# Optimization experiments

Hardware: AMD Instinct MI355X
Metric: run time of the kernel (lower is better)

## Reference

```python
import jax, jax.numpy as jnp
import numpy as np

B, IN_C, OUT_C, H, W = 16, 64, 64, 128, 128
MIN_R, MAX_R, BASE, SCALE = 1, 6, 3, 3


def setup_inputs() -> dict:
    key = jax.random.key(0)
    k1, k2 = jax.random.split(key)
    x = jax.random.normal(k1, (B, IN_C, H, W), dtype=jnp.float32)
    # kaiming-uniform-ish scale for a 3x3 conv weight
    weight = jax.random.normal(k2, (OUT_C, IN_C, 3, 3), dtype=jnp.float32) * (1.0 / np.sqrt(IN_C * 9))
    # truncated-normal-style integer dilation per output channel (deterministic)
    rng = np.random.default_rng(0)
    offsets = np.clip(np.round(rng.normal(BASE, SCALE, size=OUT_C)), MIN_R, MAX_R).astype(np.int32)
    return {"x": x, "weight": weight, "offsets": offsets}


def _gsd_conv(x, weight, offs_np):
    # Per-channel dilation conv: group channels by dilation, conv each group
    # (dilation=o, padding=o keeps HxW), scatter back to original channel order.
    out = jnp.zeros((x.shape[0], weight.shape[0], x.shape[2], x.shape[3]), dtype=x.dtype)
    for o in np.unique(offs_np):
        idx = np.nonzero(offs_np == o)[0]          # static channel indices for this dilation
        w = weight[idx]                             # [g, in_c, 3, 3]
        o = int(o)
        y = jax.lax.conv_general_dilated(
            x, w,
            window_strides=(1, 1),
            padding=[(o, o), (o, o)],
            rhs_dilation=(o, o),
            dimension_numbers=("NCHW", "OIHW", "NCHW"),
        )                                           # [B, g, H, W]
        out = out.at[:, idx].set(y)
    return out


def reference(x, weight, offsets):
    offs_np = np.asarray(offsets)
    return _gsd_conv(x, weight, offs_np)
```

## Files before the change

kernel.cpp:

```cpp
#include <hip/hip_runtime.h>


#define HW_ 128
#define C_ 64
#define B_ 16
#define EX 44
#define EY 28
#define NPIX (EY * EX)
#define PADW 140
#define MAX_ITEMS 12
#define WS_WPACK_OFF 1024
#define WS_XB16_OFF (1 << 20)
#define XB16_BYTES ((size_t)B_ * PADW * PADW * C_ * 2)


typedef __attribute__((ext_vector_type(8))) short short8;
typedef __attribute__((ext_vector_type(16))) float floatx16;

__device__ __forceinline__ unsigned bf16rne(float f) {
  unsigned u = __float_as_uint(f);
  return (u + 0x7FFFu + ((u >> 16) & 1u)) >> 16;
}

#define GLOAD_LDS16(g, l)                                   \
  __builtin_amdgcn_global_load_lds(                         \
      (const __attribute__((address_space(1))) void*)(g),   \
      (__attribute__((address_space(3))) void*)(l), 16, 0, 0)

__global__ __launch_bounds__(256) void gsd_prep(
    const float* __restrict__ x, const int* __restrict__ offsets,
    const float* __restrict__ w, int* __restrict__ desc,
    uint4* __restrict__ wpack, unsigned short* __restrict__ xb16,
    const int nrow) {
  const int bid = blockIdx.x;
  const int tid = threadIdx.x;

  if (bid < nrow) {
    const int b = bid / PADW, py = bid - b * PADW;
    uint4* o4 = (uint4*)(xb16 + (size_t)bid * (PADW * C_));
    const uint4 z = make_uint4(0, 0, 0, 0);
    if (py < 6 || py >= PADW - 6) {
      for (int i = tid; i < PADW * C_ / 8; i += 256) o4[i] = z;
      return;
    }
    if (tid < 48) o4[tid] = z;
    else if (tid < 96) o4[1024 + tid] = z;
    const int y = py - 6;
    __shared__ unsigned l32[128 * 33];
    const int xx = tid & 127, ph = tid >> 7;
    const float* xp = x + (size_t)b * (C_ * HW_ * HW_) + y * HW_ + xx;
#pragma unroll 4
    for (int p = ph; p < 32; p += 2) {
      const float v0 = xp[(2 * p) * (HW_ * HW_)];
      const float v1 = xp[(2 * p + 1) * (HW_ * HW_)];
      l32[xx * 33 + p] = bf16rne(v0) | (bf16rne(v1) << 16);
    }
    __syncthreads();
#pragma unroll 4
    for (int ch = tid; ch < 1024; ch += 256) {
      const int px = ch >> 3, qq = ch & 7;
      const unsigned* s = &l32[px * 33 + qq * 4];
      o4[48 + ch] = make_uint4(s[0], s[1], s[2], s[3]);
    }
    return;
  }

  __shared__ int sd[128];
  __shared__ int soffs[C_];
  if (tid < C_) soffs[tid] = offsets[tid];
  __syncthreads();
  if (tid < C_) {
    const int key = soffs[tid];
    int rank = 0;
    for (int c = 0; c < C_; ++c) {
      const int kc = soffs[c];
      rank += (int)((kc < key) | ((kc == key) & (c < tid)));
    }
    sd[rank] = tid;
  }
  __syncthreads();
  if (tid == 0) {
    int ni = 0;
    for (int t = 0; t < 2; ++t) {
      int cnt = 0, prev = -1;
      for (int m = 0; m < 32; ++m) {
        const int dd = soffs[sd[t * 32 + m]];
        if (dd != prev && cnt < 6 && ni < MAX_ITEMS) {
          sd[66 + t * 6 + cnt] = dd;
          sd[78 + t * 6 + cnt] = ni;
          sd[91 + ni * 2] = t;
          sd[92 + ni * 2] = dd;
          ++ni;
          ++cnt;
          prev = dd;
        }
      }
      sd[64 + t] = cnt;
    }
    sd[90] = ni;
  }
  __syncthreads();

  const int sbid = bid - nrow;
  if (sbid == 0) {
    if (tid < 91) desc[tid] = sd[tid];
    return;
  }
  const int wix = sbid - 1;
  if (wix >= sd[90]) return;
  const int o = sd[91 + wix * 2];
  const int dit = sd[92 + wix * 2];

  for (int i = tid; i < 4 * 9 * 64; i += 256) {
    const int ks = i / 576;
    const int r = i % 576;
    const int tap = r >> 6;
    const int lane = r & 63;
    const int m = lane & 31, hh = lane >> 5;
    const int oc = sd[o * 32 + m];
    const bool act = (soffs[oc] == dit);
    unsigned ww[4];
    for (int jj = 0; jj < 4; ++jj) {
      float v0 = 0.f, v1 = 0.f;
      if (act) {
        const int ic0 = ks * 16 + hh * 8 + jj * 2;
        v0 = w[(oc * C_ + ic0) * 9 + tap];
        v1 = w[(oc * C_ + ic0 + 1) * 9 + tap];
      }
      ww[jj] = bf16rne(v0) | (bf16rne(v1) << 16);
    }
    wpack[(size_t)wix * 2304 + i] = make_uint4(ww[0], ww[1], ww[2], ww[3]);
  }
}

template <bool PRE>
__global__ __launch_bounds__(512, 4) void gsd_conv(
    const float* __restrict__ x, const unsigned short* __restrict__ xb16,
    const int* __restrict__ desc, const uint4* __restrict__ wpack,
    float* __restrict__ out) {
  const int tid = threadIdx.x;
  const int gxid = blockIdx.x;
  const int b = gxid >> 5;
  const int yt = (gxid >> 2) & 7;
  const int xt = gxid & 3;
  const int y0 = yt * 16, x0 = xt * 32;

  const int lane = tid & 63;
  const int n = lane & 31;
  const int h = lane >> 5;
  const int wv = tid >> 6;
  const int o = wv >> 2;
  const int rq = wv & 3;

  __shared__ __align__(16) unsigned ldsbuf[40 * 256];

  floatx16 acc[4];
#pragma unroll
  for (int rt = 0; rt < 4; ++rt)
#pragma unroll
    for (int e = 0; e < 16; ++e) acc[rt][e] = 0.f;

  const unsigned short* xrow;
  int srcoff[5];
  if constexpr (PRE) {
    xrow = xb16 + (size_t)b * (PADW * PADW * C_);
#pragma unroll
    for (int j = 0; j < 5; ++j) {
      const int q = (wv + j * 8) * 64 + lane;
      int pix = q >> 1;
      if (pix > NPIX - 1) pix = NPIX - 1;
      const int p = q & 1;
      const int yy = pix / EX, xx = pix - yy * EX;
      const int half = p ^ ((pix >> 2) & 1);
      srcoff[j] = ((y0 + yy) * PADW + (x0 + xx)) * C_ + half * 8;
    }
  }
  int slx, sq, sy2, gxc;
  bool xin;
  const float* xb;
  if constexpr (!PRE) {
    slx = tid & 63;
    sq = (tid >> 6) & 3;
    sy2 = tid >> 8;
    xb = x + (size_t)b * (C_ * HW_ * HW_);
    const int gx = x0 - 6 + slx;
    gxc = gx < 0 ? 0 : (gx > 127 ? 127 : gx);
    xin = ((unsigned)gx < 128u) & (slx < EX);
  }

  const int cnt = __builtin_amdgcn_readfirstlane(desc[64 + o]);

  for (int ks = 0; ks < 4; ++ks) {
    if (ks) __syncthreads();
    if constexpr (PRE) {
#pragma unroll
      for (int j = 0; j < 5; ++j) {
        GLOAD_LDS16(xrow + srcoff[j] + ks * 16, &ldsbuf[(wv + j * 8) * 256]);
      }
    } else {
      const float* xp = xb + (size_t)(ks * 16 + sq * 4) * (HW_ * HW_);
#pragma unroll 2
      for (int yy = sy2; yy < EY; yy += 2) {
        const int gy = y0 - 6 + yy;
        const int gyc = gy < 0 ? 0 : (gy > 127 ? 127 : gy);
        const bool ok = xin & ((unsigned)gy < 128u);
        const float* p = xp + gyc * HW_ + gxc;
        float v0 = p[0];
        float v1 = p[HW_ * HW_];
        float v2 = p[2 * HW_ * HW_];
        float v3 = p[3 * HW_ * HW_];
        if (!ok) { v0 = v1 = v2 = v3 = 0.f; }
        const unsigned lo = bf16rne(v0) | (bf16rne(v1) << 16);
        const unsigned hi = bf16rne(v2) | (bf16rne(v3) << 16);
        if (slx < EX) {
          const int pix = yy * EX + slx;
          const int dws =
              pix * 8 + (((sq >> 1) ^ ((pix >> 2) & 1)) << 2) + ((sq & 1) << 1);
          *reinterpret_cast<uint2*>(&ldsbuf[dws]) = make_uint2(lo, hi);
        }
      }
    }
    __syncthreads();

    for (int s = 0; s < cnt; ++s) {
      const int d = __builtin_amdgcn_readfirstlane(desc[66 + o * 6 + s]);
      const int wix = __builtin_amdgcn_readfirstlane(desc[78 + o * 6 + s]);
      const uint4* wp = wpack + ((size_t)wix * 4 + ks) * 576 + lane;
#pragma unroll
      for (int tap = 0; tap < 9; ++tap) {
        const int ky = tap / 3 - 1, kx = tap % 3 - 1;
        const short8 af = __builtin_bit_cast(short8, wp[tap * 64]);
        const int pybase = rq * 4 + ky * d + 6;
        const int pxb = n + kx * d + 6;
#pragma unroll
        for (int rt = 0; rt < 4; ++rt) {
          const int pix = (pybase + rt) * EX + pxb;
          const int dws = (pix << 3) + ((h ^ ((pix >> 2) & 1)) << 2);
          const short8 bf = *reinterpret_cast<const short8*>(&ldsbuf[dws]);
          acc[rt] = __builtin_amdgcn_mfma_f32_32x32x16_bf16(af, bf, acc[rt],
                                                            0, 0, 0);
        }
      }
    }
  }

  int oc[16];
#pragma unroll
  for (int reg = 0; reg < 16; ++reg) {
    const int row = (reg & 3) + 8 * (reg >> 2) + 4 * h;
    oc[reg] = desc[o * 32 + row];
  }
#pragma unroll
  for (int rt = 0; rt < 4; ++rt) {
    const int y = y0 + rq * 4 + rt;
#pragma unroll
    for (int reg = 0; reg < 16; ++reg) {
      out[((size_t)(b * C_ + oc[reg]) * HW_ + y) * HW_ + x0 + n] =
          acc[rt][reg];
    }
  }
}

extern "C" void kernel_launch(void* const* d_in, const int* in_sizes, int n_in,
                              void* d_out, int out_size, void* d_ws,
                              size_t ws_size, hipStream_t stream) {
  const float* x = (const float*)d_in[0];
  const float* w = (const float*)d_in[1];
  const int* offsets = (const int*)d_in[2];
  float* out = (float*)d_out;

  int* desc = (int*)d_ws;
  uint4* wpack = (uint4*)((char*)d_ws + WS_WPACK_OFF);
  unsigned short* xb16 = (unsigned short*)((char*)d_ws + WS_XB16_OFF);

  const bool pre = ws_size >= (size_t)WS_XB16_OFF + XB16_BYTES;
  const int nrow = pre ? B_ * PADW : 0;

  gsd_prep<<<dim3(nrow + 1 + MAX_ITEMS), 256, 0, stream>>>(
      x, offsets, w, desc, wpack, xb16, nrow);
  if (pre) {
    gsd_conv<true><<<dim3(B_ * 8 * 4), 512, 0, stream>>>(
        x, xb16, desc, wpack, out);
  } else {
    gsd_conv<false><<<dim3(B_ * 8 * 4), 512, 0, stream>>>(
        x, xb16, desc, wpack, out);
  }
}
```

Baseline: 217.2 us.

## Double-buffer LDS staging with per-k-slice planar bf16 layout and block swizzle

Reorganizes the padded bf16 input into four 16-channel planes per batch so each k-slice load is contiguous. The conv kernel now double-buffers LDS, issuing the async global-to-LDS load for the next k-slice while computing the current one, and drops redundant chunk loads for the last set. It also remaps block IDs to change scheduling order for cache locality. Doubling LDS use (about 80KB per block) may lower occupancy below the launch-bounds target.

```diff
diff --git a/kernel.cpp b/kernel.cpp
--- a/kernel.cpp
+++ b/kernel.cpp
@@ -7,11 +7,15 @@
 #define EX 44
 #define EY 28
 #define NPIX (EY * EX)
+#define NCHUNK (NPIX * 2)
+#define NSETS 39
+#define BUFDW (NSETS * 64 * 4)
 #define PADW 140
+#define PLANE_STRIDE (PADW * PADW * 16)
 #define MAX_ITEMS 12
 #define WS_WPACK_OFF 1024
 #define WS_XB16_OFF (1 << 20)
-#define XB16_BYTES ((size_t)B_ * PADW * PADW * C_ * 2)
+#define XB16_BYTES ((size_t)B_ * 4 * PLANE_STRIDE * 2)
 
 
 typedef __attribute__((ext_vector_type(8))) short short8;
@@ -37,14 +41,21 @@
 
   if (bid < nrow) {
     const int b = bid / PADW, py = bid - b * PADW;
-    uint4* o4 = (uint4*)(xb16 + (size_t)bid * (PADW * C_));
+    uint4* o4 = (uint4*)xb16;
+    const size_t pb0 = ((size_t)b * 4) * 39200 + (size_t)py * 280;
     const uint4 z = make_uint4(0, 0, 0, 0);
     if (py < 6 || py >= PADW - 6) {
-      for (int i = tid; i < PADW * C_ / 8; i += 256) o4[i] = z;
+      for (int i = tid; i < 1120; i += 256) {
+        const int ks = i / 280, r = i - ks * 280;
+        o4[pb0 + (size_t)ks * 39200 + r] = z;
+      }
       return;
     }
-    if (tid < 48) o4[tid] = z;
-    else if (tid < 96) o4[1024 + tid] = z;
+    if (tid < 96) {
+      const int ks = tid / 24, rr = tid - ks * 24;
+      const int idx = rr < 12 ? rr : 256 + rr;
+      o4[pb0 + (size_t)ks * 39200 + idx] = z;
+    }
     const int y = py - 6;
     __shared__ unsigned l32[128 * 33];
     const int xx = tid & 127, ph = tid >> 7;
@@ -58,9 +69,9 @@
     __syncthreads();
 #pragma unroll 4
     for (int ch = tid; ch < 1024; ch += 256) {
-      const int px = ch >> 3, qq = ch & 7;
-      const unsigned* s = &l32[px * 33 + qq * 4];
-      o4[48 + ch] = make_uint4(s[0], s[1], s[2], s[3]);
+      const int ks = ch >> 8, r = ch & 255;
+      const unsigned* s = &l32[(r >> 1) * 33 + ks * 8 + (r & 1) * 4];
+      o4[pb0 + (size_t)ks * 39200 + 12 + r] = make_uint4(s[0], s[1], s[2], s[3]);
     }
     return;
   }
@@ -139,7 +150,8 @@
     const int* __restrict__ desc, const uint4* __restrict__ wpack,
     float* __restrict__ out) {
   const int tid = threadIdx.x;
-  const int gxid = blockIdx.x;
+  const int bid0 = blockIdx.x;
+  const int gxid = (bid0 & 7) * 64 + (bid0 >> 3);
   const int b = gxid >> 5;
   const int yt = (gxid >> 2) & 7;
   const int xt = gxid & 3;
@@ -152,7 +164,7 @@
   const int o = wv >> 2;
   const int rq = wv & 3;
 
-  __shared__ __align__(16) unsigned ldsbuf[40 * 256];
+  __shared__ __align__(16) unsigned ldsbuf[2][BUFDW];
 
   floatx16 acc[4];
 #pragma unroll
@@ -160,10 +172,10 @@
 #pragma unroll
     for (int e = 0; e < 16; ++e) acc[rt][e] = 0.f;
 
-  const unsigned short* xrow;
+  const unsigned short* xbase;
   int srcoff[5];
   if constexpr (PRE) {
-    xrow = xb16 + (size_t)b * (PADW * PADW * C_);
+    xbase = xb16 + (size_t)b * 4 * PLANE_STRIDE;
 #pragma unroll
     for (int j = 0; j < 5; ++j) {
       const int q = (wv + j * 8) * 64 + lane;
@@ -172,7 +184,7 @@
       const int p = q & 1;
       const int yy = pix / EX, xx = pix - yy * EX;
       const int half = p ^ ((pix >> 2) & 1);
-      srcoff[j] = ((y0 + yy) * PADW + (x0 + xx)) * C_ + half * 8;
+      srcoff[j] = ((y0 + yy) * PADW + (x0 + xx)) * 16 + half * 8;
     }
   }
   int slx, sq, sy2, gxc;
@@ -190,14 +202,56 @@
 
   const int cnt = __builtin_amdgcn_readfirstlane(desc[64 + o]);
 
-  for (int ks = 0; ks < 4; ++ks) {
-    if (ks) __syncthreads();
+  auto STAGE = [&](int buf, int ks) {
     if constexpr (PRE) {
+      const unsigned short* xp = xbase + (size_t)ks * PLANE_STRIDE;
 #pragma unroll
       for (int j = 0; j < 5; ++j) {
-        GLOAD_LDS16(xrow + srcoff[j] + ks * 16, &ldsbuf[(wv + j * 8) * 256]);
-      }
-    } else {
+        if (j < 4) {
+          GLOAD_LDS16(xp + srcoff[j], &ldsbuf[buf][(wv + j * 8) * 256]);
+        } else if (wv < 7) {
+          GLOAD_LDS16(xp + srcoff[4], &ldsbuf[buf][(wv + 32) * 256]);
+        }
+      }
+    }
+  };
+
+  auto COMPUTE = [&](const unsigned* cbuf, int ks) {
+    for (int s = 0; s < cnt; ++s) {
+      const int d = __builtin_amdgcn_readfirstlane(desc[66 + o * 6 + s]);
+      const int wix = __builtin_amdgcn_readfirstlane(desc[78 + o * 6 + s]);
+      const uint4* wp = wpack + ((size_t)wix * 4 + ks) * 576 + lane;
+#pragma unroll
+      for (int tap = 0; tap < 9; ++tap) {
+        const int ky = tap / 3 - 1, kx = tap % 3 - 1;
+        const short8 af = __builtin_bit_cast(short8, wp[tap * 64]);
+        const int pybase = rq * 4 + ky * d + 6;
+        const int pxb = n + kx * d + 6;
+#pragma unroll
+        for (int rt = 0; rt < 4; ++rt) {
+          const int pix = (pybase + rt) * EX + pxb;
+          const int dws = (pix << 3) + ((h ^ ((pix >> 2) & 1)) << 2);
+          const short8 bf = *reinterpret_cast<const short8*>(&cbuf[dws]);
+          acc[rt] = __builtin_amdgcn_mfma_f32_32x32x16_bf16(af, bf, acc[rt],
+                                                            0, 0, 0);
+        }
+      }
+    }
+  };
+
+  if constexpr (PRE) {
+    STAGE(0, 0);
+    __syncthreads();
+#pragma unroll
+    for (int ks = 0; ks < 3; ++ks) {
+      STAGE((ks + 1) & 1, ks + 1);
+      COMPUTE(ldsbuf[ks & 1], ks);
+      __syncthreads();
+    }
+    COMPUTE(ldsbuf[1], 3);
+  } else {
+    for (int ks = 0; ks < 4; ++ks) {
+      if (ks) __syncthreads();
       const float* xp = xb + (size_t)(ks * 16 + sq * 4) * (HW_ * HW_);
 #pragma unroll 2
       for (int yy = sy2; yy < EY; yy += 2) {
@@ -216,31 +270,11 @@
           const int pix = yy * EX + slx;
           const int dws =
               pix * 8 + (((sq >> 1) ^ ((pix >> 2) & 1)) << 2) + ((sq & 1) << 1);
-          *reinterpret_cast<uint2*>(&ldsbuf[dws]) = make_uint2(lo, hi);
+          *reinterpret_cast<uint2*>(&ldsbuf[0][dws]) = make_uint2(lo, hi);
         }
       }
-    }
-    __syncthreads();
-
-    for (int s = 0; s < cnt; ++s) {
-      const int d = __builtin_amdgcn_readfirstlane(desc[66 + o * 6 + s]);
-      const int wix = __builtin_amdgcn_readfirstlane(desc[78 + o * 6 + s]);
-      const uint4* wp = wpack + ((size_t)wix * 4 + ks) * 576 + lane;
-#pragma unroll
-      for (int tap = 0; tap < 9; ++tap) {
-        const int ky = tap / 3 - 1, kx = tap % 3 - 1;
-        const short8 af = __builtin_bit_cast(short8, wp[tap * 64]);
-        const int pybase = rq * 4 + ky * d + 6;
-        const int pxb = n + kx * d + 6;
-#pragma unroll
-        for (int rt = 0; rt < 4; ++rt) {
-          const int pix = (pybase + rt) * EX + pxb;
-          const int dws = (pix << 3) + ((h ^ ((pix >> 2) & 1)) << 2);
-          const short8 bf = *reinterpret_cast<const short8*>(&ldsbuf[dws]);
-          acc[rt] = __builtin_amdgcn_mfma_f32_32x32x16_bf16(af, bf, acc[rt],
-                                                            0, 0, 0);
-        }
-      }
+      __syncthreads();
+      COMPUTE(ldsbuf[0], ks);
     }
   }
 
```

Measured after the change: 185.1 us. 1.17x faster.
